# Kernel tuning notes

Hardware: AMD Instinct MI355X
Metric: run time of the kernel (lower is better)

The kernel has to match this reference:

```python
import jax, jax.numpy as jnp
import numpy as np
from jax import lax

EPS = 1e-5

# sign binarization with straight-through estimator (bitorch Sign: grad clipped to |x|<=1)
def _sign(x):
    return jnp.where(x >= 0, 1.0, -1.0).astype(x.dtype)

@jax.custom_vjp
def sign_ste(x):
    return _sign(x)

def _sign_fwd(x):
    return _sign(x), x

def _sign_bwd(x, g):
    return (g * (jnp.abs(x) <= 1.0).astype(g.dtype),)

sign_ste.defvjp(_sign_fwd, _sign_bwd)


def conv2d(x, w, stride, padding):
    return lax.conv_general_dilated(
        x, w, window_strides=(stride, stride),
        padding=[(padding, padding), (padding, padding)],
        dimension_numbers=("NCHW", "OIHW", "NCHW"))


def batchnorm(x, gamma, beta, mean, var):
    # eval-mode BN with running statistics
    inv = gamma / jnp.sqrt(var + EPS)
    return x * inv[None, :, None, None] + (beta - mean * inv)[None, :, None, None]


def avgpool2(x, stride):
    # AvgPool2d(kernel_size=2, stride=stride); here stride==2, H,W even
    B, C, H, W = x.shape
    return x.reshape(B, C, H // 2, 2, W // 2, 2).mean(axis=(3, 5))


def setup_inputs() -> dict:
    key = jax.random.key(0)
    ks = jax.random.split(key, 6)
    B, Cin, Cout, H, W = 16, 32, 64, 224, 224
    x = jax.random.normal(ks[0], (B, Cin, H, W), dtype=jnp.float32)
    w_body = jax.random.normal(ks[1], (Cout, Cin, 3, 3), dtype=jnp.float32) * 0.1
    w_ds = jax.random.normal(ks[2], (Cout, Cin, 1, 1), dtype=jnp.float32) * 0.1
    bn1_gamma = jnp.ones((Cout,), jnp.float32)
    bn1_beta = jnp.zeros((Cout,), jnp.float32)
    bn1_mean = jax.random.normal(ks[3], (Cout,), dtype=jnp.float32) * 0.1
    bn1_var = jax.random.uniform(ks[4], (Cout,), dtype=jnp.float32) + 0.5
    bn2_gamma = jnp.ones((Cout,), jnp.float32)
    bn2_beta = jnp.zeros((Cout,), jnp.float32)
    bn2_mean = jax.random.normal(ks[5], (Cout,), dtype=jnp.float32) * 0.1
    bn2_var = jax.random.uniform(jax.random.fold_in(key, 7), (Cout,), dtype=jnp.float32) + 0.5
    return dict(x=x, w_body=w_body, bn1_gamma=bn1_gamma, bn1_beta=bn1_beta,
                bn1_mean=bn1_mean, bn1_var=bn1_var, w_ds=w_ds,
                bn2_gamma=bn2_gamma, bn2_beta=bn2_beta,
                bn2_mean=bn2_mean, bn2_var=bn2_var)


def reference(x, w_body, bn1_gamma, bn1_beta, bn1_mean, bn1_var,
              w_ds, bn2_gamma, bn2_beta, bn2_mean, bn2_var):
    stride = 2
    # downsample branch (full precision): AvgPool2d(2, stride) -> 1x1 conv -> BN
    residual = avgpool2(x, stride)
    residual = conv2d(residual, w_ds, stride=1, padding=0)
    residual = batchnorm(residual, bn2_gamma, bn2_beta, bn2_mean, bn2_var)
    # body: QConv2d with sign-quantized input and weight, then BN
    xb = sign_ste(x)
    wb = sign_ste(w_body)
    body = conv2d(xb, wb, stride=stride, padding=1)
    body = batchnorm(body, bn1_gamma, bn1_beta, bn1_mean, bn1_var)
    return body + residual
```

## Files before the change

### kernel.cpp

```cpp
#include <hip/hip_runtime.h>
#include <stdint.h>

static constexpr int NB = 16;
static constexpr int CI = 32;
static constexpr int CO = 64;
static constexpr int HI = 224, WI = 224;
static constexpr int HO = 112, WO = 112;
static constexpr float EPS = 1e-5f;

typedef _Float16 h2 __attribute__((ext_vector_type(2)));

__device__ __forceinline__ h2 as_h2(uint32_t u) {
    union { uint32_t u; h2 h; } c; c.u = u; return c.h;
}
__device__ __forceinline__ uint32_t pack_h2(float a, float b) {
    union { uint32_t u; h2 h; } c;
    c.h = (h2){(_Float16)a, (_Float16)b};
    return c.u;
}

static constexpr size_t OFF_WT2 = 3072;
static constexpr size_t OFF_A1  = 7168;
static constexpr size_t OFF_CC  = 7424;
static constexpr size_t WS_NEED = 7680;

__device__ __forceinline__ int XB(int c) { return c + ((c >> 3) << 2); }
static constexpr int XBW = 132 + ((132 / 8) << 2) + 4;

__global__ __launch_bounds__(256) void prep_kernel(
    const float* __restrict__ wbody,
    const float* __restrict__ g1, const float* __restrict__ b1,
    const float* __restrict__ m1, const float* __restrict__ v1,
    const float* __restrict__ wds,
    const float* __restrict__ g2, const float* __restrict__ b2,
    const float* __restrict__ m2, const float* __restrict__ v2,
    uint32_t* __restrict__ wbits, uint32_t* __restrict__ wt2,
    float* __restrict__ A1, float* __restrict__ Cc)
{
    int i = blockIdx.x * 256 + threadIdx.x;
    if (i < 16 * CO) {
        int ci2 = i >> 6, co = i & 63;
        float inv2 = g2[co] * rsqrtf(v2[co] + EPS);
        float w0 = wds[co * CI + 2 * ci2]     * inv2;
        float w1 = wds[co * CI + 2 * ci2 + 1] * inv2;
        wt2[i] = pack_h2(w0, w1);
    } else if (i < 16 * CO + CO * 9) {
        int j = i - 16 * CO;
        int co = j / 9, k = j % 9;
        uint32_t bits = 0u;
        for (int ci = 0; ci < CI; ++ci) {
            float wv = wbody[((co * CI + ci) * 3 + (k / 3)) * 3 + (k % 3)];
            bits |= (uint32_t)(wv >= 0.0f) << ci;
        }
        wbits[co * 12 + k] = bits;
    } else if (i < 16 * CO + CO * 9 + CO) {
        int co = i - 16 * CO - CO * 9;
        float inv1 = g1[co] * rsqrtf(v1[co] + EPS);
        float inv2 = g2[co] * rsqrtf(v2[co] + EPS);
        A1[co] = -2.0f * inv1;
        Cc[co] = b1[co] - m1[co] * inv1 + b2[co] - m2[co] * inv2 + 288.0f * inv1;
    } else if (i < 16 * CO + CO * 12) {
        int j = i - 16 * CO - CO * 9 - CO + CO * 9 + CO;
        (void)j;
    }
}

__global__ __launch_bounds__(256) void fused_kernel(
    const float* __restrict__ x,
    const uint32_t* __restrict__ wbits, const uint32_t* __restrict__ wt2,
    const float* __restrict__ A1, const float* __restrict__ Cc,
    float* __restrict__ out)
{
    const int bid  = (blockIdx.x & 7) * 224 + (blockIdx.x >> 3);
    const int tile = bid & 1;
    const int gb   = bid >> 1;
    const int g    = gb % 56;
    const int b    = gb / 56;
    const int oh0  = 2 * g;
    const int ow0  = tile * 64;
    const int t    = threadIdx.x;

    __shared__ __align__(16) uint32_t s_xb[5][XBW];
    __shared__ __align__(16) uint32_t s_avg[2][16][68];
    __shared__ __align__(16) uint32_t s_wt2[16][64];
    __shared__ __align__(16) uint32_t s_wb[CO * 12];
    __shared__ float s_A1[CO], s_C[CO];

    {
        uint32_t* wt2s = (uint32_t*)s_wt2;
#pragma unroll
        for (int i = 0; i < 4; ++i) wt2s[t + 256 * i] = wt2[t + 256 * i];
#pragma unroll
        for (int i = 0; i < 3; ++i) s_wb[t + 256 * i] = wbits[t + 256 * i];
        if (t < CO) { s_A1[t] = A1[t]; s_C[t] = Cc[t]; }
    }

    {
        const int pair = t >> 7;
        const int q    = t & 3;
        const int f    = (t >> 2) & 31;
        const int jcol = 2 * ow0 + 4 * f;
        const bool colok = (jcol + 3 < WI);
        const float* xp = x + ((size_t)(b * CI + 8 * q) * HI + (2 * oh0 + 2 * pair)) * WI + jcol;
        uint32_t m0[4] = {0, 0, 0, 0}, m1r[4] = {0, 0, 0, 0};
#pragma unroll
        for (int k = 0; k < 4; ++k) {
            const int c0 = 2 * k, c1 = c0 + 1;
            const int s0 = 8 * q + 2 * k, s1 = s0 + 1;
            float4 t0 = make_float4(0.f, 0.f, 0.f, 0.f);
            float4 u0 = t0, t1 = t0, u1 = t0;
            if (colok) {
                t0 = *(const float4*)(xp + (size_t)c0 * (HI * WI));
                u0 = *(const float4*)(xp + (size_t)c0 * (HI * WI) + WI);
                t1 = *(const float4*)(xp + (size_t)c1 * (HI * WI));
                u1 = *(const float4*)(xp + (size_t)c1 * (HI * WI) + WI);
            }
            m0[0]  |= ((uint32_t)(t0.x >= 0.f) << s0) | ((uint32_t)(t1.x >= 0.f) << s1);
            m0[1]  |= ((uint32_t)(t0.y >= 0.f) << s0) | ((uint32_t)(t1.y >= 0.f) << s1);
            m0[2]  |= ((uint32_t)(t0.z >= 0.f) << s0) | ((uint32_t)(t1.z >= 0.f) << s1);
            m0[3]  |= ((uint32_t)(t0.w >= 0.f) << s0) | ((uint32_t)(t1.w >= 0.f) << s1);
            m1r[0] |= ((uint32_t)(u0.x >= 0.f) << s0) | ((uint32_t)(u1.x >= 0.f) << s1);
            m1r[1] |= ((uint32_t)(u0.y >= 0.f) << s0) | ((uint32_t)(u1.y >= 0.f) << s1);
            m1r[2] |= ((uint32_t)(u0.z >= 0.f) << s0) | ((uint32_t)(u1.z >= 0.f) << s1);
            m1r[3] |= ((uint32_t)(u0.w >= 0.f) << s0) | ((uint32_t)(u1.w >= 0.f) << s1);
            float a0p0 = 0.25f * ((t0.x + t0.y) + (u0.x + u0.y));
            float a0p1 = 0.25f * ((t0.z + t0.w) + (u0.z + u0.w));
            float a1p0 = 0.25f * ((t1.x + t1.y) + (u1.x + u1.y));
            float a1p1 = 0.25f * ((t1.z + t1.w) + (u1.z + u1.w));
            *(uint2*)&s_avg[pair][4 * q + k][2 * f] =
                make_uint2(pack_h2(a0p0, a1p0), pack_h2(a0p1, a1p1));
        }
#pragma unroll
        for (int j = 0; j < 4; ++j) {
            m0[j]  |= __shfl_xor(m0[j], 1);  m0[j]  |= __shfl_xor(m0[j], 2);
            m1r[j] |= __shfl_xor(m1r[j], 1); m1r[j] |= __shfl_xor(m1r[j], 2);
        }
        uint32_t v0  = (q == 0) ? m0[0]  : (q == 1) ? m0[1]  : (q == 2) ? m0[2]  : m0[3];
        uint32_t v1v = (q == 0) ? m1r[0] : (q == 1) ? m1r[1] : (q == 2) ? m1r[2] : m1r[3];
        s_xb[1 + 2 * pair][XB(1 + 4 * f + q)] = v0;
        s_xb[2 + 2 * pair][XB(1 + 4 * f + q)] = v1v;
    }
    if (t < 128) {
        const int q = t & 3, f = t >> 2;
        const int jcol = 2 * ow0 + 4 * f;
        uint32_t mm[4] = {0, 0, 0, 0};
        if (g > 0 && jcol + 3 < WI) {
            const float* xp = x + ((size_t)(b * CI + 8 * q) * HI + (2 * oh0 - 1)) * WI + jcol;
#pragma unroll
            for (int k = 0; k < 4; ++k) {
                const int s0 = 8 * q + 2 * k, s1 = s0 + 1;
                const float4 t0 = *(const float4*)(xp + (size_t)(2 * k) * (HI * WI));
                const float4 t1 = *(const float4*)(xp + (size_t)(2 * k + 1) * (HI * WI));
                mm[0] |= ((uint32_t)(t0.x >= 0.f) << s0) | ((uint32_t)(t1.x >= 0.f) << s1);
                mm[1] |= ((uint32_t)(t0.y >= 0.f) << s0) | ((uint32_t)(t1.y >= 0.f) << s1);
                mm[2] |= ((uint32_t)(t0.z >= 0.f) << s0) | ((uint32_t)(t1.z >= 0.f) << s1);
                mm[3] |= ((uint32_t)(t0.w >= 0.f) << s0) | ((uint32_t)(t1.w >= 0.f) << s1);
            }
        }
#pragma unroll
        for (int j = 0; j < 4; ++j) { mm[j] |= __shfl_xor(mm[j], 1); mm[j] |= __shfl_xor(mm[j], 2); }
        s_xb[0][XB(1 + 4 * f + q)] = (q == 0) ? mm[0] : (q == 1) ? mm[1] : (q == 2) ? mm[2] : mm[3];
    }
    if (t < 40) {
        const int lr = t >> 3;
        const int l  = t & 7;
        uint32_t bits = 0u;
        const int hr = 2 * oh0 - 1 + lr;
        const int wc = 2 * ow0 - 1;
        if (hr >= 0 && wc >= 0) {
            const float* xp = x + ((size_t)(b * CI + 4 * l) * HI + hr) * WI + wc;
#pragma unroll
            for (int ci = 0; ci < 4; ++ci)
                bits |= (uint32_t)(xp[(size_t)ci * (HI * WI)] >= 0.0f) << (4 * l + ci);
        }
        bits |= __shfl_xor(bits, 1);
        bits |= __shfl_xor(bits, 2);
        bits |= __shfl_xor(bits, 4);
        if (l == 0) s_xb[lr][XB(0)] = bits;
    }
    __syncthreads();

    const int cg  = t >> 4;
    const int pg  = t & 15;
    const int co0 = cg * 4;
    const int p0  = pg * 4;
    const bool pxvalid = (ow0 + p0 < WO);
    const bool px0 = (ow0 + p0 == 0);
    const int cb = 12 * pg;

#pragma unroll 1
    for (int r = 0; r < 2; ++r) {
        float fa[4][4] = {{0.f,0.f,0.f,0.f},{0.f,0.f,0.f,0.f},{0.f,0.f,0.f,0.f},{0.f,0.f,0.f,0.f}};
#pragma unroll 4
        for (int ci2 = 0; ci2 < 16; ++ci2) {
            uint4 av = *(const uint4*)&s_avg[r][ci2][p0];
            uint4 wv = *(const uint4*)&s_wt2[ci2][co0];
            h2 a[4] = {as_h2(av.x), as_h2(av.y), as_h2(av.z), as_h2(av.w)};
            h2 w[4] = {as_h2(wv.x), as_h2(wv.y), as_h2(wv.z), as_h2(wv.w)};
#pragma unroll
            for (int jc = 0; jc < 4; ++jc)
#pragma unroll
                for (int jp = 0; jp < 4; ++jp)
                    fa[jc][jp] = __builtin_amdgcn_fdot2(w[jc], a[jp], fa[jc][jp], false);
        }

        uint32_t xr[3][9];
#pragma unroll
        for (int rI = 0; rI < 3; ++rI) {
            const uint32_t* row = s_xb[2 * r + rI];
            uint4 a  = *(const uint4*)&row[cb];
            uint4 bq = *(const uint4*)&row[cb + 4];
            xr[rI][0] = a.x;  xr[rI][1] = a.y;  xr[rI][2] = a.z;  xr[rI][3] = a.w;
            xr[rI][4] = bq.x; xr[rI][5] = bq.y; xr[rI][6] = bq.z; xr[rI][7] = bq.w;
            xr[rI][8] = row[cb + 12];
        }

        const bool oh0f = (g == 0 && r == 0);

        int sfin[4][4];
#pragma unroll
        for (int jc = 0; jc < 4; ++jc) {
            const int co = co0 + jc;
            uint4 wa  = *(const uint4*)&s_wb[co * 12];
            uint4 wb4 = *(const uint4*)&s_wb[co * 12 + 4];
            uint32_t wv[9] = {wa.x, wa.y, wa.z, wa.w, wb4.x, wb4.y, wb4.z, wb4.w,
                              s_wb[co * 12 + 8]};
#pragma unroll
            for (int jp = 0; jp < 4; ++jp) {
                int c00 = __popc(xr[0][2 * jp + 0] ^ wv[0]);
                int c01 = __popc(xr[0][2 * jp + 1] ^ wv[1]);
                int c02 = __popc(xr[0][2 * jp + 2] ^ wv[2]);
                int c10 = __popc(xr[1][2 * jp + 0] ^ wv[3]);
                int c11 = __popc(xr[1][2 * jp + 1] ^ wv[4]);
                int c12 = __popc(xr[1][2 * jp + 2] ^ wv[5]);
                int c20 = __popc(xr[2][2 * jp + 0] ^ wv[6]);
                int c21 = __popc(xr[2][2 * jp + 1] ^ wv[7]);
                int c22 = __popc(xr[2][2 * jp + 2] ^ wv[8]);
                int r0v  = c00 + c01 + c02;
                int ssum = r0v + c10 + c11 + c12 + c20 + c21 + c22;
                if (oh0f) ssum += 48 - r0v;
                if (px0 && jp == 0) {
                    ssum += 48 - (c00 + c10 + c20);
                    if (oh0f) ssum += c00 - 16;
                }
                sfin[jc][jp] = ssum;
            }
        }

        if (pxvalid) {
#pragma unroll
            for (int jc = 0; jc < 4; ++jc) {
                const int co = co0 + jc;
                const float n2a = s_A1[co], cc = s_C[co];
                float4 o;
                o.x = fmaf(n2a, (float)sfin[jc][0], fa[jc][0] + cc);
                o.y = fmaf(n2a, (float)sfin[jc][1], fa[jc][1] + cc);
                o.z = fmaf(n2a, (float)sfin[jc][2], fa[jc][2] + cc);
                o.w = fmaf(n2a, (float)sfin[jc][3], fa[jc][3] + cc);
                *(float4*)&out[((size_t)(b * CO + co) * HO + (oh0 + r)) * WO + ow0 + p0] = o;
            }
        }
    }
}

__global__ __launch_bounds__(256) void naive_kernel(
    const float* __restrict__ x, const float* __restrict__ wbody,
    const float* __restrict__ g1, const float* __restrict__ b1,
    const float* __restrict__ m1, const float* __restrict__ v1,
    const float* __restrict__ wds,
    const float* __restrict__ g2, const float* __restrict__ b2,
    const float* __restrict__ m2, const float* __restrict__ v2,
    float* __restrict__ out)
{
    int i = blockIdx.x * 256 + threadIdx.x;
    if (i >= NB * CO * HO * WO) return;
    int ow = i % WO;
    int oh = (i / WO) % HO;
    int co = (i / (WO * HO)) % CO;
    int b  = i / (WO * HO * CO);
    float inv1 = g1[co] * rsqrtf(v1[co] + EPS);
    float inv2 = g2[co] * rsqrtf(v2[co] + EPS);
    int body = 0;
    float ds = 0.f;
    for (int ci = 0; ci < CI; ++ci) {
        const float* xp = x + (size_t)(b * CI + ci) * (HI * WI);
        for (int kh = 0; kh < 3; ++kh) {
            int hh = 2 * oh - 1 + kh;
            if (hh < 0 || hh >= HI) continue;
            for (int kw = 0; kw < 3; ++kw) {
                int ww = 2 * ow - 1 + kw;
                if (ww < 0 || ww >= WI) continue;
                float xv = xp[(size_t)hh * WI + ww];
                float wv = wbody[((co * CI + ci) * 3 + kh) * 3 + kw];
                int sx = (xv >= 0.f) ? 1 : -1;
                int sw = (wv >= 0.f) ? 1 : -1;
                body += sx * sw;
            }
        }
        float a = 0.25f * (xp[(size_t)(2 * oh) * WI + 2 * ow]
                         + xp[(size_t)(2 * oh) * WI + 2 * ow + 1]
                         + xp[(size_t)(2 * oh + 1) * WI + 2 * ow]
                         + xp[(size_t)(2 * oh + 1) * WI + 2 * ow + 1]);
        ds += a * wds[co * CI + ci];
    }
    out[i] = inv1 * (float)body + (b1[co] - m1[co] * inv1)
           + inv2 * ds + (b2[co] - m2[co] * inv2);
}

extern "C" void kernel_launch(void* const* d_in, const int* in_sizes, int n_in,
                              void* d_out, int out_size, void* d_ws, size_t ws_size,
                              hipStream_t stream)
{
    (void)in_sizes; (void)n_in; (void)out_size;
    const float* x   = (const float*)d_in[0];
    const float* wbd = (const float*)d_in[1];
    const float* g1  = (const float*)d_in[2];
    const float* b1  = (const float*)d_in[3];
    const float* m1  = (const float*)d_in[4];
    const float* v1  = (const float*)d_in[5];
    const float* wds = (const float*)d_in[6];
    const float* g2  = (const float*)d_in[7];
    const float* b2  = (const float*)d_in[8];
    const float* m2  = (const float*)d_in[9];
    const float* v2  = (const float*)d_in[10];
    float* out = (float*)d_out;

    if (ws_size < WS_NEED) {
        int total = NB * CO * HO * WO;
        naive_kernel<<<(total + 255) / 256, 256, 0, stream>>>(
            x, wbd, g1, b1, m1, v1, wds, g2, b2, m2, v2, out);
        return;
    }

    char* wsb = (char*)d_ws;
    uint32_t* wbits = (uint32_t*)wsb;
    uint32_t* wt2   = (uint32_t*)(wsb + OFF_WT2);
    float*    A1    = (float*)(wsb + OFF_A1);
    float*    Cc    = (float*)(wsb + OFF_CC);

    prep_kernel<<<7, 256, 0, stream>>>(wbd, g1, b1, m1, v1, wds, g2, b2, m2, v2,
                                       wbits, wt2, A1, Cc);
    fused_kernel<<<dim3(NB * 56 * 2), 256, 0, stream>>>(
        x, wbits, wt2, A1, Cc, out);
}
```

Baseline: 49.59 us.

## Process four output rows per block and prefetch next rows during compute

Each block now covers four output rows instead of two, which halves the grid and the per-block weight staging and halo loads. The input rows for the second pair of output rows are loaded into registers while the first two rows are being computed, so global load latency is hidden behind the popcount and fdot2 work. The cost is more shared memory and registers per block and fewer blocks, which may reduce occupancy and wave balance.

```diff
diff --git a/kernel.cpp b/kernel.cpp
--- a/kernel.cpp
+++ b/kernel.cpp
@@ -6,6 +6,7 @@
 static constexpr int CO = 64;
 static constexpr int HI = 224, WI = 224;
 static constexpr int HO = 112, WO = 112;
+static constexpr int HW = HI * WI;
 static constexpr float EPS = 1e-5f;
 
 typedef _Float16 h2 __attribute__((ext_vector_type(2)));
@@ -49,7 +50,7 @@
         int co = j / 9, k = j % 9;
         uint32_t bits = 0u;
         for (int ci = 0; ci < CI; ++ci) {
-            float wv = wbody[((co * CI + ci) * 3 + (k / 3)) * 3 + (k % 3)];
+            float wv = wbody[(co * CI + ci) * 9 + k];
             bits |= (uint32_t)(wv >= 0.0f) << ci;
         }
         wbits[co * 12 + k] = bits;
@@ -59,29 +60,26 @@
         float inv2 = g2[co] * rsqrtf(v2[co] + EPS);
         A1[co] = -2.0f * inv1;
         Cc[co] = b1[co] - m1[co] * inv1 + b2[co] - m2[co] * inv2 + 288.0f * inv1;
-    } else if (i < 16 * CO + CO * 12) {
-        int j = i - 16 * CO - CO * 9 - CO + CO * 9 + CO;
-        (void)j;
     }
 }
 
 __global__ __launch_bounds__(256) void fused_kernel(
     const float* __restrict__ x,
     const uint32_t* __restrict__ wbits, const uint32_t* __restrict__ wt2,
-    const float* __restrict__ A1, const float* __restrict__ Cc,
+    const float* __restrict__ A1p, const float* __restrict__ Ccp,
     float* __restrict__ out)
 {
-    const int bid  = (blockIdx.x & 7) * 224 + (blockIdx.x >> 3);
+    const int bid  = (blockIdx.x & 7) * 112 + (blockIdx.x >> 3);
     const int tile = bid & 1;
     const int gb   = bid >> 1;
-    const int g    = gb % 56;
-    const int b    = gb / 56;
-    const int oh0  = 2 * g;
+    const int gg   = gb % 28;
+    const int b    = gb / 28;
+    const int ih0  = 8 * gg;
     const int ow0  = tile * 64;
     const int t    = threadIdx.x;
 
-    __shared__ __align__(16) uint32_t s_xb[5][XBW];
-    __shared__ __align__(16) uint32_t s_avg[2][16][68];
+    __shared__ __align__(16) uint32_t s_xb[9][XBW];
+    __shared__ __align__(16) uint32_t s_avg[4][16][68];
     __shared__ __align__(16) uint32_t s_wt2[16][64];
     __shared__ __align__(16) uint32_t s_wb[CO * 12];
     __shared__ float s_A1[CO], s_C[CO];
@@ -92,16 +90,17 @@
         for (int i = 0; i < 4; ++i) wt2s[t + 256 * i] = wt2[t + 256 * i];
 #pragma unroll
         for (int i = 0; i < 3; ++i) s_wb[t + 256 * i] = wbits[t + 256 * i];
-        if (t < CO) { s_A1[t] = A1[t]; s_C[t] = Cc[t]; }
-    }
+        if (t < CO) { s_A1[t] = A1p[t]; s_C[t] = Ccp[t]; }
+    }
+
+    const int pair = t >> 7;
+    const int q    = t & 3;
+    const int f    = (t >> 2) & 31;
+    const int jcol = 2 * ow0 + 4 * f;
+    const bool colok = (jcol + 3 < WI);
 
     {
-        const int pair = t >> 7;
-        const int q    = t & 3;
-        const int f    = (t >> 2) & 31;
-        const int jcol = 2 * ow0 + 4 * f;
-        const bool colok = (jcol + 3 < WI);
-        const float* xp = x + ((size_t)(b * CI + 8 * q) * HI + (2 * oh0 + 2 * pair)) * WI + jcol;
+        const float* xp = x + ((size_t)(b * CI + 8 * q) * HI + (ih0 + 2 * pair)) * WI + jcol;
         uint32_t m0[4] = {0, 0, 0, 0}, m1r[4] = {0, 0, 0, 0};
 #pragma unroll
         for (int k = 0; k < 4; ++k) {
@@ -110,10 +109,10 @@
             float4 t0 = make_float4(0.f, 0.f, 0.f, 0.f);
             float4 u0 = t0, t1 = t0, u1 = t0;
             if (colok) {
-                t0 = *(const float4*)(xp + (size_t)c0 * (HI * WI));
-                u0 = *(const float4*)(xp + (size_t)c0 * (HI * WI) + WI);
-                t1 = *(const float4*)(xp + (size_t)c1 * (HI * WI));
-                u1 = *(const float4*)(xp + (size_t)c1 * (HI * WI) + WI);
+                t0 = *(const float4*)(xp + (size_t)c0 * HW);
+                u0 = *(const float4*)(xp + (size_t)c0 * HW + WI);
+                t1 = *(const float4*)(xp + (size_t)c1 * HW);
+                u1 = *(const float4*)(xp + (size_t)c1 * HW + WI);
             }
             m0[0]  |= ((uint32_t)(t0.x >= 0.f) << s0) | ((uint32_t)(t1.x >= 0.f) << s1);
             m0[1]  |= ((uint32_t)(t0.y >= 0.f) << s0) | ((uint32_t)(t1.y >= 0.f) << s1);
@@ -141,16 +140,16 @@
         s_xb[2 + 2 * pair][XB(1 + 4 * f + q)] = v1v;
     }
     if (t < 128) {
-        const int q = t & 3, f = t >> 2;
-        const int jcol = 2 * ow0 + 4 * f;
+        const int hq = t & 3, hf = t >> 2;
+        const int hj = 2 * ow0 + 4 * hf;
         uint32_t mm[4] = {0, 0, 0, 0};
-        if (g > 0 && jcol + 3 < WI) {
-            const float* xp = x + ((size_t)(b * CI + 8 * q) * HI + (2 * oh0 - 1)) * WI + jcol;
+        if (gg > 0 && hj + 3 < WI) {
+            const float* xp = x + ((size_t)(b * CI + 8 * hq) * HI + (ih0 - 1)) * WI + hj;
 #pragma unroll
             for (int k = 0; k < 4; ++k) {
-                const int s0 = 8 * q + 2 * k, s1 = s0 + 1;
-                const float4 t0 = *(const float4*)(xp + (size_t)(2 * k) * (HI * WI));
-                const float4 t1 = *(const float4*)(xp + (size_t)(2 * k + 1) * (HI * WI));
+                const int s0 = 8 * hq + 2 * k, s1 = s0 + 1;
+                const float4 t0 = *(const float4*)(xp + (size_t)(2 * k) * HW);
+                const float4 t1 = *(const float4*)(xp + (size_t)(2 * k + 1) * HW);
                 mm[0] |= ((uint32_t)(t0.x >= 0.f) << s0) | ((uint32_t)(t1.x >= 0.f) << s1);
                 mm[1] |= ((uint32_t)(t0.y >= 0.f) << s0) | ((uint32_t)(t1.y >= 0.f) << s1);
                 mm[2] |= ((uint32_t)(t0.z >= 0.f) << s0) | ((uint32_t)(t1.z >= 0.f) << s1);
@@ -159,19 +158,18 @@
         }
 #pragma unroll
         for (int j = 0; j < 4; ++j) { mm[j] |= __shfl_xor(mm[j], 1); mm[j] |= __shfl_xor(mm[j], 2); }
-        s_xb[0][XB(1 + 4 * f + q)] = (q == 0) ? mm[0] : (q == 1) ? mm[1] : (q == 2) ? mm[2] : mm[3];
+        s_xb[0][XB(1 + 4 * hf + hq)] = (hq == 0) ? mm[0] : (hq == 1) ? mm[1] : (hq == 2) ? mm[2] : mm[3];
     }
     if (t < 40) {
-        const int lr = t >> 3;
-        const int l  = t & 7;
+        const int lr = t >> 3, l = t & 7;
         uint32_t bits = 0u;
-        const int hr = 2 * oh0 - 1 + lr;
+        const int hr = ih0 - 1 + lr;
         const int wc = 2 * ow0 - 1;
         if (hr >= 0 && wc >= 0) {
             const float* xp = x + ((size_t)(b * CI + 4 * l) * HI + hr) * WI + wc;
 #pragma unroll
             for (int ci = 0; ci < 4; ++ci)
-                bits |= (uint32_t)(xp[(size_t)ci * (HI * WI)] >= 0.0f) << (4 * l + ci);
+                bits |= (uint32_t)(xp[(size_t)ci * HW] >= 0.0f) << (4 * l + ci);
         }
         bits |= __shfl_xor(bits, 1);
         bits |= __shfl_xor(bits, 2);
@@ -188,8 +186,7 @@
     const bool px0 = (ow0 + p0 == 0);
     const int cb = 12 * pg;
 
-#pragma unroll 1
-    for (int r = 0; r < 2; ++r) {
+    auto compute_row = [&](int r) {
         float fa[4][4] = {{0.f,0.f,0.f,0.f},{0.f,0.f,0.f,0.f},{0.f,0.f,0.f,0.f},{0.f,0.f,0.f,0.f}};
 #pragma unroll 4
         for (int ci2 = 0; ci2 < 16; ++ci2) {
@@ -203,7 +200,6 @@
                 for (int jp = 0; jp < 4; ++jp)
                     fa[jc][jp] = __builtin_amdgcn_fdot2(w[jc], a[jp], fa[jc][jp], false);
         }
-
         uint32_t xr[3][9];
 #pragma unroll
         for (int rI = 0; rI < 3; ++rI) {
@@ -214,9 +210,7 @@
             xr[rI][4] = bq.x; xr[rI][5] = bq.y; xr[rI][6] = bq.z; xr[rI][7] = bq.w;
             xr[rI][8] = row[cb + 12];
         }
-
-        const bool oh0f = (g == 0 && r == 0);
-
+        const bool ohf = (gg == 0 && r == 0);
         int sfin[4][4];
 #pragma unroll
         for (int jc = 0; jc < 4; ++jc) {
@@ -238,15 +232,14 @@
                 int c22 = __popc(xr[2][2 * jp + 2] ^ wv[8]);
                 int r0v  = c00 + c01 + c02;
                 int ssum = r0v + c10 + c11 + c12 + c20 + c21 + c22;
-                if (oh0f) ssum += 48 - r0v;
+                if (ohf) ssum += 48 - r0v;
                 if (px0 && jp == 0) {
                     ssum += 48 - (c00 + c10 + c20);
-                    if (oh0f) ssum += c00 - 16;
+                    if (ohf) ssum += c00 - 16;
                 }
                 sfin[jc][jp] = ssum;
             }
         }
-
         if (pxvalid) {
 #pragma unroll
             for (int jc = 0; jc < 4; ++jc) {
@@ -257,10 +250,104 @@
                 o.y = fmaf(n2a, (float)sfin[jc][1], fa[jc][1] + cc);
                 o.z = fmaf(n2a, (float)sfin[jc][2], fa[jc][2] + cc);
                 o.w = fmaf(n2a, (float)sfin[jc][3], fa[jc][3] + cc);
-                *(float4*)&out[((size_t)(b * CO + co) * HO + (oh0 + r)) * WO + ow0 + p0] = o;
+                *(float4*)&out[((size_t)(b * CO + co) * HO + (4 * gg + r)) * WO + ow0 + p0] = o;
             }
         }
-    }
+    };
+
+    const float* xp2 = x + ((size_t)(b * CI + 8 * q) * HI + (ih0 + 4 + 2 * pair)) * WI + jcol;
+    uint32_t n0[4] = {0, 0, 0, 0}, n1[4] = {0, 0, 0, 0};
+
+    auto proc_k = [&](int k, const float4& t0, const float4& u0,
+                      const float4& t1, const float4& u1) {
+        const int s0 = 8 * q + 2 * k, s1 = s0 + 1;
+        n0[0] |= ((uint32_t)(t0.x >= 0.f) << s0) | ((uint32_t)(t1.x >= 0.f) << s1);
+        n0[1] |= ((uint32_t)(t0.y >= 0.f) << s0) | ((uint32_t)(t1.y >= 0.f) << s1);
+        n0[2] |= ((uint32_t)(t0.z >= 0.f) << s0) | ((uint32_t)(t1.z >= 0.f) << s1);
+        n0[3] |= ((uint32_t)(t0.w >= 0.f) << s0) | ((uint32_t)(t1.w >= 0.f) << s1);
+        n1[0] |= ((uint32_t)(u0.x >= 0.f) << s0) | ((uint32_t)(u1.x >= 0.f) << s1);
+        n1[1] |= ((uint32_t)(u0.y >= 0.f) << s0) | ((uint32_t)(u1.y >= 0.f) << s1);
+        n1[2] |= ((uint32_t)(u0.z >= 0.f) << s0) | ((uint32_t)(u1.z >= 0.f) << s1);
+        n1[3] |= ((uint32_t)(u0.w >= 0.f) << s0) | ((uint32_t)(u1.w >= 0.f) << s1);
+        float a0p0 = 0.25f * ((t0.x + t0.y) + (u0.x + u0.y));
+        float a0p1 = 0.25f * ((t0.z + t0.w) + (u0.z + u0.w));
+        float a1p0 = 0.25f * ((t1.x + t1.y) + (u1.x + u1.y));
+        float a1p1 = 0.25f * ((t1.z + t1.w) + (u1.z + u1.w));
+        *(uint2*)&s_avg[2 + pair][4 * q + k][2 * f] =
+            make_uint2(pack_h2(a0p0, a1p0), pack_h2(a0p1, a1p1));
+    };
+
+    float4 cA[8];
+#pragma unroll
+    for (int k = 0; k < 2; ++k) {
+        float4 z = make_float4(0.f, 0.f, 0.f, 0.f);
+        cA[4*k] = z; cA[4*k+1] = z; cA[4*k+2] = z; cA[4*k+3] = z;
+        if (colok) {
+            cA[4*k+0] = *(const float4*)(xp2 + (size_t)(2 * k) * HW);
+            cA[4*k+1] = *(const float4*)(xp2 + (size_t)(2 * k) * HW + WI);
+            cA[4*k+2] = *(const float4*)(xp2 + (size_t)(2 * k + 1) * HW);
+            cA[4*k+3] = *(const float4*)(xp2 + (size_t)(2 * k + 1) * HW + WI);
+        }
+    }
+
+    compute_row(0);
+
+    proc_k(0, cA[0], cA[1], cA[2], cA[3]);
+    proc_k(1, cA[4], cA[5], cA[6], cA[7]);
+
+    float4 cB[8];
+#pragma unroll
+    for (int k = 0; k < 2; ++k) {
+        float4 z = make_float4(0.f, 0.f, 0.f, 0.f);
+        cB[4*k] = z; cB[4*k+1] = z; cB[4*k+2] = z; cB[4*k+3] = z;
+        if (colok) {
+            cB[4*k+0] = *(const float4*)(xp2 + (size_t)(2 * k + 4) * HW);
+            cB[4*k+1] = *(const float4*)(xp2 + (size_t)(2 * k + 4) * HW + WI);
+            cB[4*k+2] = *(const float4*)(xp2 + (size_t)(2 * k + 5) * HW);
+            cB[4*k+3] = *(const float4*)(xp2 + (size_t)(2 * k + 5) * HW + WI);
+        }
+    }
+    float hv[4] = {1.f, 1.f, 1.f, 1.f};
+    const int wc = 2 * ow0 - 1;
+    if (t < 32 && wc >= 0) {
+        const int lr = t >> 3, l = t & 7;
+        const float* xp = x + ((size_t)(b * CI + 4 * l) * HI + (ih0 + 4 + lr)) * WI + wc;
+#pragma unroll
+        for (int ci = 0; ci < 4; ++ci) hv[ci] = xp[(size_t)ci * HW];
+    }
+
+    compute_row(1);
+
+    proc_k(2, cB[0], cB[1], cB[2], cB[3]);
+    proc_k(3, cB[4], cB[5], cB[6], cB[7]);
+#pragma unroll
+    for (int j = 0; j < 4; ++j) {
+        n0[j] |= __shfl_xor(n0[j], 1); n0[j] |= __shfl_xor(n0[j], 2);
+        n1[j] |= __shfl_xor(n1[j], 1); n1[j] |= __shfl_xor(n1[j], 2);
+    }
+    {
+        uint32_t v0  = (q == 0) ? n0[0] : (q == 1) ? n0[1] : (q == 2) ? n0[2] : n0[3];
+        uint32_t v1v = (q == 0) ? n1[0] : (q == 1) ? n1[1] : (q == 2) ? n1[2] : n1[3];
+        s_xb[5 + 2 * pair][XB(1 + 4 * f + q)] = v0;
+        s_xb[6 + 2 * pair][XB(1 + 4 * f + q)] = v1v;
+    }
+    if (t < 32) {
+        const int lr = t >> 3, l = t & 7;
+        uint32_t bits = 0u;
+        if (wc >= 0) {
+#pragma unroll
+            for (int ci = 0; ci < 4; ++ci)
+                bits |= (uint32_t)(hv[ci] >= 0.0f) << (4 * l + ci);
+        }
+        bits |= __shfl_xor(bits, 1);
+        bits |= __shfl_xor(bits, 2);
+        bits |= __shfl_xor(bits, 4);
+        if (l == 0) s_xb[5 + lr][XB(0)] = bits;
+    }
+    __syncthreads();
+
+    compute_row(2);
+    compute_row(3);
 }
 
 __global__ __launch_bounds__(256) void naive_kernel(
@@ -283,7 +370,7 @@
     int body = 0;
     float ds = 0.f;
     for (int ci = 0; ci < CI; ++ci) {
-        const float* xp = x + (size_t)(b * CI + ci) * (HI * WI);
+        const float* xp = x + (size_t)(b * CI + ci) * HW;
         for (int kh = 0; kh < 3; ++kh) {
             int hh = 2 * oh - 1 + kh;
             if (hh < 0 || hh >= HI) continue;
@@ -340,6 +427,6 @@
 
     prep_kernel<<<7, 256, 0, stream>>>(wbd, g1, b1, m1, v1, wds, g2, b2, m2, v2,
                                        wbits, wt2, A1, Cc);
-    fused_kernel<<<dim3(NB * 56 * 2), 256, 0, stream>>>(
+    fused_kernel<<<dim3(NB * 28 * 2), 256, 0, stream>>>(
         x, wbits, wt2, A1, Cc, out);
 }
```

Result: slower. 55.66 us (+12.2%).
